# Optimization experiments

Hardware: AMD Instinct MI355X
Metric: run time of the kernel (lower is better)

Reference implementation:

```python
import jax, jax.numpy as jnp
import numpy as np

EMBED_DIM = 1024
NUM_HEADS = 16
HEAD_WIDTH = 64  # EMBED_DIM == NUM_HEADS * HEAD_WIDTH
B, L = 2, 1024


def setup_inputs() -> dict:
    key = jax.random.key(0)
    ks = jax.random.split(key, 7)
    s = EMBED_DIM ** -0.5
    return {
        "x": jax.random.normal(ks[0], (B, L, EMBED_DIM), dtype=jnp.float32),
        "bias": jax.random.normal(ks[1], (B, L, L, NUM_HEADS), dtype=jnp.float32),
        # nn.Linear weights are (out_features, in_features)
        "w_proj": jax.random.normal(ks[2], (3 * EMBED_DIM, EMBED_DIM), dtype=jnp.float32) * s,
        "w_o": jax.random.normal(ks[3], (EMBED_DIM, EMBED_DIM), dtype=jnp.float32) * s,
        "b_o": jnp.zeros((EMBED_DIM,), dtype=jnp.float32),
        "w_g": jax.random.normal(ks[4], (EMBED_DIM, EMBED_DIM), dtype=jnp.float32) * s,
        "b_g": jnp.ones((EMBED_DIM,), dtype=jnp.float32),
    }


def reference(x, bias, w_proj, w_o, b_o, w_g, b_g):
    b, l, e = x.shape
    h, hw = NUM_HEADS, HEAD_WIDTH
    # fused QKV projection: (B,L,3E) -> (B,H,L,3*hw), head-major split as in torch
    t = jnp.einsum('ble,fe->blf', x, w_proj)
    t = t.reshape(b, l, h, 3 * hw).transpose(0, 2, 1, 3)  # (B,H,L,3hw)
    q, k, v = jnp.split(t, 3, axis=-1)
    q = q * (hw ** -0.5)
    a = jnp.einsum('bhqc,bhkc->bhqk', q, k)
    a = a + bias.transpose(0, 3, 1, 2)  # bias: (B,Lq,Lk,H) -> (B,H,Lq,Lk)
    a = jax.nn.softmax(a, axis=-1)
    y = jnp.einsum('bhqk,bhkc->bqhc', a, v).reshape(b, l, e)
    g = jax.nn.sigmoid(jnp.einsum('ble,fe->blf', x, w_g) + b_g)
    y = g * y
    y = jnp.einsum('ble,fe->blf', y, w_o) + b_o
    # faithful to original rearrange('... lq lk h -> ... h lq lk') applied to (B,h,lq,lk):
    attn = jnp.transpose(a, (0, 3, 1, 2))  # (B, lk, h, lq)
    return y, attn
```

## Files before the change

### kernel.cpp

```cpp
#include <hip/hip_runtime.h>
#include <hip/hip_bf16.h>
#include <stdint.h>

typedef __attribute__((ext_vector_type(4))) float f32x4;
typedef __attribute__((ext_vector_type(8))) short short8;
typedef __attribute__((ext_vector_type(4))) unsigned short u16x4;
typedef unsigned short us;

#define DEV __device__ __forceinline__
#define MFMA16(a, b, c) __builtin_amdgcn_mfma_f32_16x16x32_bf16(a, b, c, 0, 0, 0)

DEV us f2b(float x) {
  union { float f; uint32_t u; } c; c.f = x;
  uint32_t r = (c.u + 0x7fffu + ((c.u >> 16) & 1u)) >> 16;
  return (us)r;
}
DEV float b2f(us x) {
  union { uint32_t u; float f; } c; c.u = ((uint32_t)x) << 16;
  return c.f;
}

DEV void gload_lds16(const void* g, void* l) {
  __builtin_amdgcn_global_load_lds((const __attribute__((address_space(1))) void*)g,
                                   (__attribute__((address_space(3))) void*)l, 16, 0, 0);
}

__global__ __launch_bounds__(256) void prep_k(
    const float* __restrict__ x, const float* __restrict__ wproj,
    const float* __restrict__ wg, const float* __restrict__ wo,
    us* __restrict__ Xbf, us* __restrict__ Wbf, us* __restrict__ Wobf) {
  int i = blockIdx.x * 256 + threadIdx.x;
  const float* src; us* dst;
  if (i < 524288)               { src = x     + (size_t)i * 4;                  dst = Xbf + (size_t)i * 4; }
  else if (i < 524288 + 786432) { int j = i - 524288;            src = wproj + (size_t)j * 4; dst = Wbf + (size_t)j * 4; }
  else if (i < 524288 + 786432 + 262144) { int j = i - (524288 + 786432); src = wg + (size_t)j * 4; dst = Wbf + 3145728 + (size_t)j * 4; }
  else                          { int j = i - (524288 + 786432 + 262144); src = wo + (size_t)j * 4; dst = Wobf + (size_t)j * 4; }
  f32x4 v = *(const f32x4*)src;
  u16x4 o; o.x = f2b(v.x); o.y = f2b(v.y); o.z = f2b(v.z); o.w = f2b(v.w);
  *(u16x4*)dst = o;
}

DEV void gemm_stage(char* sm, const us* A, const us* Bw,
                    int tileMrow, int tileNrow, int buf, int kt, int lane, int wid) {
  const char* gA = (const char*)A;
  const char* gB = (const char*)Bw;
#pragma unroll
  for (int i = 0; i < 2; ++i) {
    int c = wid * 2 + i;
    int off = c * 1024 + lane * 16;
    int r = off >> 6, cb = off & 63;
    gload_lds16(gA + ((size_t)(tileMrow + r) * 2048) + kt * 64 + cb, sm + buf * 8192 + c * 1024);
    gload_lds16(gB + ((size_t)(tileNrow + r) * 2048) + kt * 64 + cb, sm + 16384 + buf * 8192 + c * 1024);
  }
}

DEV void gemm_main(const us* A, const us* Bw,
                   int tileMrow, int tileNrow, f32x4 acc[4][4], char* sm) {
  int tid = threadIdx.x, lane = tid & 63, wid = tid >> 6;
  int wr = wid >> 1, wc = wid & 1;
  gemm_stage(sm, A, Bw, tileMrow, tileNrow, 0, 0, lane, wid);
  for (int kt = 0; kt < 32; ++kt) {
    __syncthreads();
    if (kt < 31) gemm_stage(sm, A, Bw, tileMrow, tileNrow, (kt + 1) & 1, kt + 1, lane, wid);
    int ab = (kt & 1) * 8192;
    int rb = (lane & 15) * 64 + ((lane >> 4) * 16);
    short8 af[4], bf[4];
#pragma unroll
    for (int mi = 0; mi < 4; ++mi)
      af[mi] = *(const short8*)(sm + ab + (wr * 64 + mi * 16) * 64 + rb);
#pragma unroll
    for (int ni = 0; ni < 4; ++ni)
      bf[ni] = *(const short8*)(sm + 16384 + ab + (wc * 64 + ni * 16) * 64 + rb);
#pragma unroll
    for (int mi = 0; mi < 4; ++mi)
#pragma unroll
      for (int ni = 0; ni < 4; ++ni)
        acc[mi][ni] = MFMA16(af[mi], bf[ni], acc[mi][ni]);
  }
}

__global__ __launch_bounds__(256) void gemm_qkvg_k(
    const us* __restrict__ Xbf, const us* __restrict__ Wbf,
    us* __restrict__ Qb, us* __restrict__ Kb, us* __restrict__ Vt,
    float* __restrict__ G, const float* __restrict__ bg) {
  __shared__ char sm[32768];
  int bid = blockIdx.x;
  int swz = (bid & 7) * 64 + (bid >> 3);
  int tileM = swz >> 5, tileN = swz & 31;
  f32x4 acc[4][4] = {};
  gemm_main(Xbf, Wbf, tileM * 128, tileN * 128, acc, sm);
  int lane = threadIdx.x & 63, wid = threadIdx.x >> 6;
  int wr = wid >> 1, wc = wid & 1;
#pragma unroll
  for (int mi = 0; mi < 4; ++mi)
#pragma unroll
    for (int ni = 0; ni < 4; ++ni)
#pragma unroll
      for (int j = 0; j < 4; ++j) {
        int row = tileM * 128 + wr * 64 + mi * 16 + ((lane >> 4) << 2) + j;
        int col = tileN * 128 + wc * 64 + ni * 16 + (lane & 15);
        float v = acc[mi][ni][j];
        int b = row >> 10, l = row & 1023;
        if (col < 3072) {
          int h = col / 192, r = col - h * 192;
          size_t base = ((size_t)(b * 16 + h) * 1024 + l) * 64;
          if (r < 64)        Qb[base + r] = f2b(v * 0.125f);
          else if (r < 128)  Kb[base + (r - 64)] = f2b(v);
          else               Vt[((size_t)(b * 16 + h) * 64 + (r - 128)) * 1024 + l] = f2b(v);
        } else {
          int e = col - 3072;
          float s = v + bg[e];
          G[(size_t)row * 1024 + e] = 1.f / (1.f + __expf(-s));
        }
      }
}

__global__ __launch_bounds__(512, 4) void qke_k(
    const us* __restrict__ Qb, const us* __restrict__ Kb,
    const float* __restrict__ bias, us* __restrict__ E,
    float* __restrict__ lpart) {
  __shared__ float bt[2][8704];
  int tid = threadIdx.x, lane = tid & 63, w = tid >> 6;
  int la = lane & 15, lg = lane >> 4;
  int bid = blockIdx.x;
  int grp = bid & 7, qt = bid >> 3;
  int b = grp >> 2, kc = grp & 3;
  int lq0 = qt * 16, lk00 = kc * 256;
  int h0 = w * 2;

  short8 qf[2][2];
#pragma unroll
  for (int t = 0; t < 2; ++t) {
    size_t bh = (size_t)(b * 16 + h0 + t);
#pragma unroll
    for (int ks = 0; ks < 2; ++ks)
      qf[t][ks] = *(const short8*)(Qb + bh * 65536 + (size_t)(lq0 + la) * 64 + ks * 32 + lg * 8);
  }

  const float* bsrc = bias + ((size_t)b << 24) + ((size_t)lq0 << 14);
#pragma unroll
  for (int i = 0; i < 4; ++i) {
    int f = i * 512 + tid;
    int h4 = f & 3, lk = (f >> 2) & 31, q = f >> 7;
    f32x4 v = *(const f32x4*)(bsrc + ((size_t)q << 14) + ((size_t)(lk00 + lk) << 4) + h4 * 4);
    float* d = &bt[0][(q * 32 + lk) * 17 + h4 * 4];
    d[0] = v.x; d[1] = v.y; d[2] = v.z; d[3] = v.w;
  }

  float lacc[2] = {0.f, 0.f};
#pragma unroll 1
  for (int sc = 0; sc < 8; ++sc) {
    __syncthreads();
    if (sc < 7) {
      int lkg2 = lk00 + (sc + 1) * 32;
      float* bd = bt[(sc + 1) & 1];
#pragma unroll
      for (int i = 0; i < 4; ++i) {
        int f = i * 512 + tid;
        int h4 = f & 3, lk = (f >> 2) & 31, q = f >> 7;
        f32x4 v = *(const f32x4*)(bsrc + ((size_t)q << 14) + ((size_t)(lkg2 + lk) << 4) + h4 * 4);
        float* d = &bd[(q * 32 + lk) * 17 + h4 * 4];
        d[0] = v.x; d[1] = v.y; d[2] = v.z; d[3] = v.w;
      }
    }
    const float* btc = bt[sc & 1];
    int lkg = lk00 + sc * 32;
#pragma unroll
    for (int t = 0; t < 2; ++t) {
      int h = h0 + t;
      const us* Kh = Kb + (size_t)(b * 16 + h) * 65536;
#pragma unroll
      for (int fr = 0; fr < 2; ++fr) {
        const us* kr = Kh + (size_t)(lkg + fr * 16 + la) * 64 + lg * 8;
        short8 kf0 = *(const short8*)kr;
        short8 kf1 = *(const short8*)(kr + 32);
        f32x4 a;
#pragma unroll
        for (int j = 0; j < 4; ++j)
          a[j] = btc[(la * 32 + fr * 16 + lg * 4 + j) * 17 + h];
        a = MFMA16(kf0, qf[t][0], a);
        a = MFMA16(kf1, qf[t][1], a);
        u16x4 ev;
#pragma unroll
        for (int j = 0; j < 4; ++j) {
          float e = __expf(a[j]);
          lacc[t] += e;
          ev[j] = f2b(e);
        }
        *(u16x4*)(E + (((size_t)(b * 1024 + lq0 + la) * 16 + h) << 10) + lkg + fr * 16 + lg * 4) = ev;
      }
    }
  }
#pragma unroll
  for (int t = 0; t < 2; ++t) {
    float s = lacc[t];
    s += __shfl_xor(s, 16);
    s += __shfl_xor(s, 32);
    if (lg == 0) lpart[kc * 32768 + (b * 16 + h0 + t) * 1024 + lq0 + la] = s;
  }
}

__global__ __launch_bounds__(256) void pv_k(
    const us* __restrict__ E, const us* __restrict__ Vt,
    const float* __restrict__ lpart, const float* __restrict__ G,
    float* __restrict__ outa, us* __restrict__ Ybf) {
  __shared__ char sm[49792];
  float* lv = (float*)(sm + 49664);
  int tid = threadIdx.x, lane = tid & 63, w = tid >> 6;
  int la = lane & 15, lg = lane >> 4;
  int bid = blockIdx.x;
  int g = bid >> 8, qt = (bid >> 3) & 31, xx = bid & 7;
  int bh = g * 8 + xx;
  int b = bh >> 4, h = bh & 15;
  int qb = qt * 32;
  if (tid < 32) {
    int r = bh * 1024 + qb + tid;
    float s = lpart[r] + lpart[32768 + r] + lpart[65536 + r] + lpart[98304 + r];
    lv[tid] = 1.f / s;
  }
  __syncthreads();
  char* pb = sm + w * 4096;
  const us* Vh = Vt + (size_t)bh * 65536;
  f32x4 yacc[2][4] = {};
  int lkw = w * 256;

#pragma unroll 1
  for (int cc = 0; cc < 4; ++cc) {
    int lk0 = lkw + cc * 64;
#pragma unroll
    for (int it = 0; it < 4; ++it) {
      int ci = it * 64 + lane;
      int q = ci >> 3, c16 = ci & 7;
      short8 ev = *(const short8*)(E + (((size_t)(b * 1024 + qb + q) * 16 + h) << 10) + lk0 + c16 * 8);
      *(short8*)(pb + q * 128 + ((c16 * 16) ^ ((q & 7) << 4))) = ev;
    }
#pragma unroll
    for (int it = 0; it < 8; ++it) {
      int idx = it * 64 + lane;
      int lkL = idx >> 3, q4 = idx & 7;
      f32x4 ov;
#pragma unroll
      for (int i = 0; i < 4; ++i) {
        int q = q4 * 4 + i;
        us e = *(const us*)(pb + q * 128 + ((2 * lkL) ^ ((q & 7) << 4)));
        ov[i] = b2f(e) * lv[q];
      }
      *(f32x4*)(outa + (((size_t)(b * 1024 + lk0 + lkL) * 16 + h) << 10) + qb + q4 * 4) = ov;
    }
#pragma unroll
    for (int ks = 0; ks < 2; ++ks) {
      short8 pa[2];
#pragma unroll
      for (int qh = 0; qh < 2; ++qh) {
        int row = qh * 16 + la;
        pa[qh] = *(const short8*)(pb + row * 128 + ((ks * 64 + lg * 16) ^ ((row & 7) << 4)));
      }
#pragma unroll
      for (int ni = 0; ni < 4; ++ni) {
        short8 vf = *(const short8*)(Vh + (size_t)(ni * 16 + la) * 1024 + lk0 + ks * 32 + lg * 8);
        yacc[0][ni] = MFMA16(pa[0], vf, yacc[0][ni]);
        yacc[1][ni] = MFMA16(pa[1], vf, yacc[1][ni]);
      }
    }
  }

  float* red = (float*)(sm + 16384);
#pragma unroll
  for (int qh = 0; qh < 2; ++qh)
#pragma unroll
    for (int ni = 0; ni < 4; ++ni)
#pragma unroll
      for (int j = 0; j < 4; ++j) {
        int r = qh * 16 + lg * 4 + j, c = ni * 16 + la;
        red[w * 2080 + r * 65 + c] = yacc[qh][ni][j];
      }
  __syncthreads();
#pragma unroll
  for (int rr = 0; rr < 8; ++rr) {
    int e = rr * 256 + tid;
    int r = e >> 6, c = e & 63;
    float s = red[r * 65 + c] + red[2080 + r * 65 + c] +
              red[4160 + r * 65 + c] + red[6240 + r * 65 + c];
    size_t gi = (((size_t)(b * 1024 + qb + r)) << 10) + h * 64 + c;
    Ybf[gi] = f2b(s * lv[r] * G[gi]);
  }
}

__global__ __launch_bounds__(256) void gemm_out_k(
    const us* __restrict__ Ybf, const us* __restrict__ Wobf,
    const float* __restrict__ bo, float* __restrict__ outy) {
  __shared__ char sm[32768];
  int bid = blockIdx.x;
  int swz = (bid & 7) * 16 + (bid >> 3);
  int tileM = swz >> 3, tileN = swz & 7;
  f32x4 acc[4][4] = {};
  gemm_main(Ybf, Wobf, tileM * 128, tileN * 128, acc, sm);
  int lane = threadIdx.x & 63, wid = threadIdx.x >> 6;
  int wr = wid >> 1, wc = wid & 1;
#pragma unroll
  for (int mi = 0; mi < 4; ++mi)
#pragma unroll
    for (int ni = 0; ni < 4; ++ni)
#pragma unroll
      for (int j = 0; j < 4; ++j) {
        int row = tileM * 128 + wr * 64 + mi * 16 + ((lane >> 4) << 2) + j;
        int col = tileN * 128 + wc * 64 + ni * 16 + (lane & 15);
        outy[(size_t)row * 1024 + col] = acc[mi][ni][j] + bo[col];
      }
}

extern "C" void kernel_launch(void* const* d_in, const int* in_sizes, int n_in,
                              void* d_out, int out_size, void* d_ws, size_t ws_size,
                              hipStream_t stream) {
  const float* x     = (const float*)d_in[0];
  const float* bias  = (const float*)d_in[1];
  const float* wproj = (const float*)d_in[2];
  const float* wo    = (const float*)d_in[3];
  const float* bo    = (const float*)d_in[4];
  const float* wg    = (const float*)d_in[5];
  const float* bg    = (const float*)d_in[6];
  float* outy = (float*)d_out;
  float* outa = outy + 2097152;

  char* ws = (char*)d_ws;
  us*    Xbf  = (us*)(ws);
  us*    Wbf  = (us*)(ws + 4  * 1024 * 1024);
  us*    Wobf = (us*)(ws + 12 * 1024 * 1024);
  us*    Qb   = (us*)(ws + 14 * 1024 * 1024);
  us*    Kb   = (us*)(ws + 18 * 1024 * 1024);
  us*    Vt   = (us*)(ws + 22 * 1024 * 1024);
  float* G    = (float*)(ws + 26 * 1024 * 1024);
  us*    Ybf  = (us*)(ws + 34 * 1024 * 1024);
  float* lpart= (float*)(ws + (size_t)38 * 1024 * 1024);
  us*    E    = (us*)   (ws + (size_t)40 * 1024 * 1024);
  if (ws_size < (size_t)104 * 1024 * 1024) return;

  prep_k<<<dim3(7168), dim3(256), 0, stream>>>(x, wproj, wg, wo, Xbf, Wbf, Wobf);
  gemm_qkvg_k<<<dim3(512), dim3(256), 0, stream>>>(Xbf, Wbf, Qb, Kb, Vt, G, bg);
  qke_k<<<dim3(512), dim3(512), 0, stream>>>(Qb, Kb, bias, E, lpart);
  pv_k<<<dim3(1024), dim3(256), 0, stream>>>(E, Vt, lpart, G, outa, Ybf);
  gemm_out_k<<<dim3(128), dim3(256), 0, stream>>>(Ybf, Wobf, bo, outy);
}
```

Baseline: 203.2 us.

## Restructure QK·bias kernel with per-wave direct-to-LDS bias loads and finer row-sum partials

The bias+QK^T+exp kernel is reorganised so each of 4 waves owns a 64-key slice and loops over all 16 heads. It loads bias tiles straight into LDS with global_load_lds instead of staging through registers, and drops the block-wide syncs. Row-sum partials are now written per 16-key fragment, 64 partials instead of 4, and pv_k sums all 64. The workspace layout is enlarged to hold them. In exchange, Q fragments are reloaded per head and loop iteration, lpart traffic grows, and each bias load waits fully on vmcnt with no double buffering.

```diff
diff --git a/kernel.cpp b/kernel.cpp
--- a/kernel.cpp
+++ b/kernel.cpp
@@ -115,88 +115,70 @@
       }
 }
 
-__global__ __launch_bounds__(512, 4) void qke_k(
+__global__ __launch_bounds__(256) void qke_k(
     const us* __restrict__ Qb, const us* __restrict__ Kb,
     const float* __restrict__ bias, us* __restrict__ E,
     float* __restrict__ lpart) {
-  __shared__ float bt[2][8704];
+  __shared__ float bt[4][16][260];
   int tid = threadIdx.x, lane = tid & 63, w = tid >> 6;
   int la = lane & 15, lg = lane >> 4;
   int bid = blockIdx.x;
-  int grp = bid & 7, qt = bid >> 3;
-  int b = grp >> 2, kc = grp & 3;
-  int lq0 = qt * 16, lk00 = kc * 256;
-  int h0 = w * 2;
-
-  short8 qf[2][2];
-#pragma unroll
-  for (int t = 0; t < 2; ++t) {
-    size_t bh = (size_t)(b * 16 + h0 + t);
-#pragma unroll
-    for (int ks = 0; ks < 2; ++ks)
-      qf[t][ks] = *(const short8*)(Qb + bh * 65536 + (size_t)(lq0 + la) * 64 + ks * 32 + lg * 8);
-  }
-
+  int b = (bid & 7) >> 2, kc = bid & 3;
+  int qt = bid >> 3;
+  int lq0 = qt * 16;
+  int lkw = kc * 256 + w * 64;
+  float* bw = &bt[w][0][0];
   const float* bsrc = bias + ((size_t)b << 24) + ((size_t)lq0 << 14);
-#pragma unroll
-  for (int i = 0; i < 4; ++i) {
-    int f = i * 512 + tid;
-    int h4 = f & 3, lk = (f >> 2) & 31, q = f >> 7;
-    f32x4 v = *(const f32x4*)(bsrc + ((size_t)q << 14) + ((size_t)(lk00 + lk) << 4) + h4 * 4);
-    float* d = &bt[0][(q * 32 + lk) * 17 + h4 * 4];
-    d[0] = v.x; d[1] = v.y; d[2] = v.z; d[3] = v.w;
-  }
-
-  float lacc[2] = {0.f, 0.f};
+
 #pragma unroll 1
-  for (int sc = 0; sc < 8; ++sc) {
-    __syncthreads();
-    if (sc < 7) {
-      int lkg2 = lk00 + (sc + 1) * 32;
-      float* bd = bt[(sc + 1) & 1];
-#pragma unroll
-      for (int i = 0; i < 4; ++i) {
-        int f = i * 512 + tid;
-        int h4 = f & 3, lk = (f >> 2) & 31, q = f >> 7;
-        f32x4 v = *(const f32x4*)(bsrc + ((size_t)q << 14) + ((size_t)(lkg2 + lk) << 4) + h4 * 4);
-        float* d = &bd[(q * 32 + lk) * 17 + h4 * 4];
-        d[0] = v.x; d[1] = v.y; d[2] = v.z; d[3] = v.w;
-      }
-    }
-    const float* btc = bt[sc & 1];
-    int lkg = lk00 + sc * 32;
-#pragma unroll
-    for (int t = 0; t < 2; ++t) {
-      int h = h0 + t;
-      const us* Kh = Kb + (size_t)(b * 16 + h) * 65536;
-#pragma unroll
-      for (int fr = 0; fr < 2; ++fr) {
-        const us* kr = Kh + (size_t)(lkg + fr * 16 + la) * 64 + lg * 8;
+  for (int fo = 0; fo < 4; ++fo) {
+    int lkf = lkw + fo * 16;
+    asm volatile("s_waitcnt lgkmcnt(0)" ::: "memory");
+#pragma unroll
+    for (int q = 0; q < 16; ++q)
+      gload_lds16((const char*)(bsrc + ((size_t)q << 14) + ((size_t)lkf << 4)) + lane * 16,
+                  (char*)(bw + q * 260));
+    asm volatile("s_waitcnt vmcnt(0)" ::: "memory");
+#pragma unroll 1
+    for (int hp = 0; hp < 8; ++hp) {
+      float lacc[2];
+#pragma unroll
+      for (int s = 0; s < 2; ++s) {
+        int h = hp * 2 + s;
+        size_t bh = (size_t)(b * 16 + h);
+        const us* Qh = Qb + bh * 65536;
+        const us* Kh = Kb + bh * 65536;
+        short8 qf0 = *(const short8*)(Qh + (size_t)(lq0 + la) * 64 + lg * 8);
+        short8 qf1 = *(const short8*)(Qh + (size_t)(lq0 + la) * 64 + 32 + lg * 8);
+        const us* kr = Kh + (size_t)(lkf + la) * 64 + lg * 8;
         short8 kf0 = *(const short8*)kr;
         short8 kf1 = *(const short8*)(kr + 32);
         f32x4 a;
 #pragma unroll
         for (int j = 0; j < 4; ++j)
-          a[j] = btc[(la * 32 + fr * 16 + lg * 4 + j) * 17 + h];
-        a = MFMA16(kf0, qf[t][0], a);
-        a = MFMA16(kf1, qf[t][1], a);
+          a[j] = bw[la * 260 + (lg * 4 + j) * 16 + h];
+        a = MFMA16(kf0, qf0, a);
+        a = MFMA16(kf1, qf1, a);
         u16x4 ev;
+        float l = 0.f;
 #pragma unroll
         for (int j = 0; j < 4; ++j) {
           float e = __expf(a[j]);
-          lacc[t] += e;
+          l += e;
           ev[j] = f2b(e);
         }
-        *(u16x4*)(E + (((size_t)(b * 1024 + lq0 + la) * 16 + h) << 10) + lkg + fr * 16 + lg * 4) = ev;
+        lacc[s] = l;
+        *(u16x4*)(E + (((size_t)(b * 1024 + lq0 + la) * 16 + h) << 10) + lkf + lg * 4) = ev;
+      }
+      int g = kc * 16 + w * 4 + fo;
+#pragma unroll
+      for (int s = 0; s < 2; ++s) {
+        float v = lacc[s];
+        v += __shfl_xor(v, 16);
+        v += __shfl_xor(v, 32);
+        if (lg == 0) lpart[(size_t)g * 32768 + (b * 16 + hp * 2 + s) * 1024 + lq0 + la] = v;
       }
     }
-  }
-#pragma unroll
-  for (int t = 0; t < 2; ++t) {
-    float s = lacc[t];
-    s += __shfl_xor(s, 16);
-    s += __shfl_xor(s, 32);
-    if (lg == 0) lpart[kc * 32768 + (b * 16 + h0 + t) * 1024 + lq0 + la] = s;
   }
 }
 
@@ -215,7 +197,9 @@
   int qb = qt * 32;
   if (tid < 32) {
     int r = bh * 1024 + qb + tid;
-    float s = lpart[r] + lpart[32768 + r] + lpart[65536 + r] + lpart[98304 + r];
+    float s = 0.f;
+#pragma unroll
+    for (int gg = 0; gg < 64; ++gg) s += lpart[(size_t)gg * 32768 + r];
     lv[tid] = 1.f / s;
   }
   __syncthreads();
@@ -332,12 +316,12 @@
   float* G    = (float*)(ws + 26 * 1024 * 1024);
   us*    Ybf  = (us*)(ws + 34 * 1024 * 1024);
   float* lpart= (float*)(ws + (size_t)38 * 1024 * 1024);
-  us*    E    = (us*)   (ws + (size_t)40 * 1024 * 1024);
-  if (ws_size < (size_t)104 * 1024 * 1024) return;
+  us*    E    = (us*)   (ws + (size_t)48 * 1024 * 1024);
+  if (ws_size < (size_t)112 * 1024 * 1024) return;
 
   prep_k<<<dim3(7168), dim3(256), 0, stream>>>(x, wproj, wg, wo, Xbf, Wbf, Wobf);
   gemm_qkvg_k<<<dim3(512), dim3(256), 0, stream>>>(Xbf, Wbf, Qb, Kb, Vt, G, bg);
-  qke_k<<<dim3(512), dim3(512), 0, stream>>>(Qb, Kb, bias, E, lpart);
+  qke_k<<<dim3(512), dim3(256), 0, stream>>>(Qb, Kb, bias, E, lpart);
   pv_k<<<dim3(1024), dim3(256), 0, stream>>>(E, Vt, lpart, G, outa, Ybf);
   gemm_out_k<<<dim3(128), dim3(256), 0, stream>>>(Ybf, Wobf, bo, outy);
 }
```

After: 248.3 us. 22.2% more time.
